# Optimization experiments

Measured on AMD Instinct MI355X. Metric: run time of the kernel, lower is better.

## Reference

```python
import jax, jax.numpy as jnp
import numpy as np

N = 100_000   # active voxels
CIN = 64
COUT = 64
K = 3
L = 128       # voxel grid extent per axis
C = K // 2    # kernel center


def _offsets():
    # spatial offsets (z, y, x) for all non-center kernel taps, in the same
    # enumeration order as the original module's triple loop
    offs = []
    for dz in range(K):
        for dy in range(K):
            for dx in range(K):
                if (dz, dy, dx) != (C, C, C):
                    offs.append((dz - C, dy - C, dx - C))
    return offs


def _build_neighbor_map(coords):
    # coords: [N,3] int, unique. For each offset build (out_idx, in_idx) pairs
    # where voxel out_idx has an active neighbor in_idx at coords+offset.
    keys = (coords[:, 0].astype(np.int64) * L + coords[:, 1]) * L + coords[:, 2]
    order = np.argsort(keys)
    skeys = keys[order]
    pairs = []
    for (z, y, x) in _offsets():
        nb = coords + np.array([z, y, x], dtype=coords.dtype)
        valid = np.all((nb >= 0) & (nb < L), axis=1)
        nkeys = (nb[:, 0].astype(np.int64) * L + nb[:, 1]) * L + nb[:, 2]
        pos = np.clip(np.searchsorted(skeys, nkeys), 0, N - 1)
        found = valid & (skeys[pos] == nkeys)
        out_idx = np.nonzero(found)[0].astype(np.int32)
        in_idx = order[pos[found]].astype(np.int32)
        pairs.append((out_idx, in_idx))
    P = max(len(o) for o, _ in pairs)
    nei = np.zeros((len(pairs), P, 2), dtype=np.int32)
    sizes = np.zeros(len(pairs), dtype=np.int32)
    for i, (o, j) in enumerate(pairs):
        nei[i, :len(o), 0] = o
        nei[i, :len(o), 1] = j
        sizes[i] = len(o)
    return nei, sizes


def setup_inputs() -> dict:
    rng = np.random.default_rng(0)
    flat = rng.choice(L * L * L, size=N, replace=False)  # unique voxel coords
    coords = np.stack([flat // (L * L), (flat // L) % L, flat % L], axis=1).astype(np.int32)
    nei, sizes = _build_neighbor_map(coords)
    key = jax.random.key(0)
    k1, k2, k3 = jax.random.split(key, 3)
    sp_values = jax.random.normal(k1, (N, CIN), dtype=jnp.float32)
    weight = jax.random.normal(k2, (COUT, K, K, K, CIN), dtype=jnp.float32) * 0.05
    bias = jax.random.normal(k3, (COUT,), dtype=jnp.float32)
    return {"sp_values": sp_values, "weight": weight, "bias": bias,
            "nei_indices": jnp.asarray(nei), "nei_sizes": jnp.asarray(sizes)}


def reference(sp_values, weight, bias, nei_indices, nei_sizes):
    # weight: [Cout,kz,ky,kx,Cin] -> [kz,ky,kx,Cin,Cout] (matches torch permute)
    w = jnp.transpose(weight, (1, 2, 3, 4, 0))
    out = sp_values @ w[C, C, C]                                   # center tap: [N,Cout]
    offs = _offsets()
    w_offs = jnp.stack([w[z + C, y + C, x + C] for (z, y, x) in offs])  # [O,Cin,Cout]
    P = nei_indices.shape[1]
    valid = (jnp.arange(P)[None, :] < nei_sizes[:, None]).astype(sp_values.dtype)  # [O,P]
    gathered = sp_values[nei_indices[:, :, 1]] * valid[:, :, None]  # [O,P,Cin], padded rows zeroed
    contrib = jnp.einsum('opc,ocd->opd', gathered, w_offs)          # [O,P,Cout]
    out = out.at[nei_indices[:, :, 0].reshape(-1)].add(contrib.reshape(-1, out.shape[1]))
    return out + bias
```

## Files before the change

### kernel.cpp

```cpp
#include <hip/hip_runtime.h>


typedef __bf16 bf16x8 __attribute__((ext_vector_type(8)));
typedef float f32x4 __attribute__((ext_vector_type(4)));

__device__ __forceinline__ unsigned short f2bf(float f) {
    union { float f; unsigned int u; } v; v.f = f;
    unsigned int u = v.u;
    return (unsigned short)((u + 0x7FFFu + ((u >> 16) & 1u)) >> 16);
}

__device__ __forceinline__ ushort4 cvt4(float4 v) {
    ushort4 b;
    b.x = f2bf(v.x); b.y = f2bf(v.y); b.z = f2bf(v.z); b.w = f2bf(v.w);
    return b;
}

__global__ __launch_bounds__(256) void sp3d_prep(
    const float* __restrict__ sp, const float* __restrict__ w,
    unsigned short* __restrict__ spb, unsigned short* __restrict__ wb,
    int* __restrict__ tbl, int n_rows)
{
    const long gt = (long)blockIdx.x * 256 + threadIdx.x;
    const long stride = (long)gridDim.x * 256;

    const long ntbl = 26L * n_rows;
    for (long i = gt; i < (ntbl >> 2); i += stride)
        *(int4*)&tbl[i * 4] = make_int4(-1, -1, -1, -1);
    if (gt < (ntbl & 3)) tbl[(ntbl & ~3L) + gt] = -1;

    const long nsp = (long)n_rows * 16;
    for (long i = gt; i < nsp; i += stride) {
        float4 v = *(const float4*)&sp[i * 4];
        *(ushort4*)&spb[i * 4] = cvt4(v);
    }

    for (long i = gt; i < 27 * 512; i += stride) {
        int tap = (int)(i >> 9);
        int rem = (int)(i & 511);
        int fragid = rem >> 6, lane = rem & 63;
        int nt = fragid >> 1, half = fragid & 1, ml = lane & 15, quad = lane >> 4;
        const float* src = w + (nt * 16 + ml) * 1728 + tap * 64 + half * 32 + quad * 8;
        float4 v0 = *(const float4*)src;
        float4 v1 = *(const float4*)(src + 4);
        *(ushort4*)&wb[i * 8]     = cvt4(v0);
        *(ushort4*)&wb[i * 8 + 4] = cvt4(v1);
    }
}

__global__ __launch_bounds__(256) void sp3d_build(
    const int* __restrict__ nei, const int* __restrict__ sizes,
    int* __restrict__ tbl, int n_rows, int P)
{
    const int o = blockIdx.y;
    const int p = blockIdx.x * 256 + threadIdx.x;
    if (p < sizes[o]) {
        int2 pr = *(const int2*)&nei[(o * P + p) * 2];
        tbl[(long)o * n_rows + pr.x] = pr.y;
    }
}

__global__ __launch_bounds__(512) void sp3d_main(
    const unsigned short* __restrict__ spb, const unsigned short* __restrict__ wb,
    const float* __restrict__ bias, const int* __restrict__ tbl,
    float* __restrict__ out, int n_rows)
{
    __shared__ unsigned short Bt[2][4096];
    __shared__ int tl[26 * 128];

    const int t = threadIdx.x;
    const int row0 = blockIdx.x * 128;
    const int wid = t >> 6, lane = t & 63, ml = lane & 15, quad = lane >> 4;

    for (int i = t; i < 26 * 128; i += 512) {
        int o = i >> 7;
        int r = row0 + (i & 127);
        tl[i] = tbl[(long)o * n_rows + (r < n_rows ? r : n_rows - 1)];
    }
    *(bf16x8*)&Bt[0][t * 8] = *(const bf16x8*)(wb + t * 8);

    bf16x8 z8;
    #pragma unroll
    for (int j = 0; j < 8; ++j) z8[j] = (__bf16)0.f;

    int curv = tl[wid * 16 + ml];
    bf16x8 a0 = z8, a1 = z8;
    if (curv >= 0) {
        const unsigned short* ap = spb + (long)curv * 64 + quad * 8;
        a0 = *(const bf16x8*)ap;
        a1 = *(const bf16x8*)(ap + 32);
    }

    f32x4 acc[4];
    #pragma unroll
    for (int nt = 0; nt < 4; ++nt) acc[nt] = f32x4{0.f, 0.f, 0.f, 0.f};

    __syncthreads();

    int cur = 0;
    for (int tp = 0; tp < 27; ++tp) {
        bf16x8 s0 = z8;
        if (tp < 26) s0 = *(const bf16x8*)(wb + (tp + 1) * 4096 + t * 8);

        int ninr = -1;
        bf16x8 na0 = z8, na1 = z8;
        if (tp < 26) {
            int tn = tp + 1;
            if (tn == 13) {
                int r = row0 + wid * 16 + ml;
                ninr = (r < n_rows) ? r : n_rows - 1;
            } else {
                int o = tn - (tn > 13 ? 1 : 0);
                ninr = tl[o * 128 + wid * 16 + ml];
            }
            if (ninr >= 0) {
                const unsigned short* ap = spb + (long)ninr * 64 + quad * 8;
                na0 = *(const bf16x8*)ap;
                na1 = *(const bf16x8*)(ap + 32);
            }
        }

        if (__any(curv >= 0)) {
            #pragma unroll
            for (int nt = 0; nt < 4; ++nt) {
                bf16x8 b0 = *(const bf16x8*)&Bt[cur][(nt * 2 + 0) * 512 + lane * 8];
                bf16x8 b1 = *(const bf16x8*)&Bt[cur][(nt * 2 + 1) * 512 + lane * 8];
                acc[nt] = __builtin_amdgcn_mfma_f32_16x16x32_bf16(a0, b0, acc[nt], 0, 0, 0);
                acc[nt] = __builtin_amdgcn_mfma_f32_16x16x32_bf16(a1, b1, acc[nt], 0, 0, 0);
            }
        }

        if (tp < 26) *(bf16x8*)&Bt[cur ^ 1][t * 8] = s0;
        __syncthreads();
        a0 = na0; a1 = na1; curv = ninr;
        cur ^= 1;
    }

    #pragma unroll
    for (int nt = 0; nt < 4; ++nt) {
        int col = nt * 16 + ml;
        float bv = bias[col];
        #pragma unroll
        for (int rg = 0; rg < 4; ++rg) {
            int row = row0 + wid * 16 + quad * 4 + rg;
            if (row < n_rows) out[(long)row * 64 + col] = acc[nt][rg] + bv;
        }
    }
}

extern "C" void kernel_launch(void* const* d_in, const int* in_sizes, int n_in,
                              void* d_out, int out_size, void* d_ws, size_t ws_size,
                              hipStream_t stream) {
    const float* sp    = (const float*)d_in[0];
    const float* w     = (const float*)d_in[1];
    const float* bias  = (const float*)d_in[2];
    const int*   nei   = (const int*)d_in[3];
    const int*   sizes = (const int*)d_in[4];
    float* out = (float*)d_out;

    const int N = in_sizes[0] / 64;
    const int P = in_sizes[3] / (26 * 2);

    char* ws = (char*)d_ws;
    unsigned short* spb = (unsigned short*)ws;
    size_t off = ((size_t)N * 64 * 2 + 255) & ~(size_t)255;
    unsigned short* wb = (unsigned short*)(ws + off);
    off = (off + 27 * 4096 * 2 + 255) & ~(size_t)255;
    int* tbl = (int*)(ws + off);

    sp3d_prep<<<dim3(2048), 256, 0, stream>>>(sp, w, spb, wb, tbl, N);
    sp3d_build<<<dim3((P + 255) / 256, 26), 256, 0, stream>>>(nei, sizes, tbl, N, P);
    sp3d_main<<<dim3((N + 127) / 128), 512, 0, stream>>>(spb, wb, bias, tbl, out, N);
}
```

Before: 133.0 us.

## Split output channels across grid, preload all tap weights to LDS, deepen gather prefetch

The main kernel grid gains a second dimension of 4 that splits the 64 output channels into 16-column blocks. Each block now preloads its slice of all 27 tap weights into shared memory once, which removes the per-tap double-buffered weight loads and __syncthreads. The gathered activation rows are prefetched two taps ahead instead of one. The cost is that every neighbor row is gathered four times, once per channel block, so gather traffic rises fourfold in exchange for more blocks and fewer barriers.

```diff
diff --git a/kernel.cpp b/kernel.cpp
--- a/kernel.cpp
+++ b/kernel.cpp
@@ -65,86 +65,83 @@
     const float* __restrict__ bias, const int* __restrict__ tbl,
     float* __restrict__ out, int n_rows)
 {
-    __shared__ unsigned short Bt[2][4096];
+    __shared__ unsigned short Bt[27 * 1024];
     __shared__ int tl[26 * 128];
 
     const int t = threadIdx.x;
     const int row0 = blockIdx.x * 128;
+    const int cb = blockIdx.y;
     const int wid = t >> 6, lane = t & 63, ml = lane & 15, quad = lane >> 4;
+    const int mrow = wid * 16 + ml;
 
+    for (int j = t; j < 27 * 128; j += 512) {
+        int tap = j >> 7, rem = j & 127;
+        *(bf16x8*)&Bt[j * 8] = *(const bf16x8*)(wb + tap * 4096 + cb * 1024 + rem * 8);
+    }
     for (int i = t; i < 26 * 128; i += 512) {
         int o = i >> 7;
         int r = row0 + (i & 127);
         tl[i] = tbl[(long)o * n_rows + (r < n_rows ? r : n_rows - 1)];
     }
-    *(bf16x8*)&Bt[0][t * 8] = *(const bf16x8*)(wb + t * 8);
+    __syncthreads();
 
     bf16x8 z8;
     #pragma unroll
     for (int j = 0; j < 8; ++j) z8[j] = (__bf16)0.f;
 
-    int curv = tl[wid * 16 + ml];
-    bf16x8 a0 = z8, a1 = z8;
-    if (curv >= 0) {
-        const unsigned short* ap = spb + (long)curv * 64 + quad * 8;
-        a0 = *(const bf16x8*)ap;
-        a1 = *(const bf16x8*)(ap + 32);
+    f32x4 acc = f32x4{0.f, 0.f, 0.f, 0.f};
+
+    int v0, v1;
+    bf16x8 a0 = z8, a1 = z8, na0 = z8, na1 = z8;
+    {
+        v0 = tl[mrow];
+        if (v0 >= 0) {
+            const unsigned short* ap = spb + (long)v0 * 64 + quad * 8;
+            a0 = *(const bf16x8*)ap; a1 = *(const bf16x8*)(ap + 32);
+        }
+        v1 = tl[128 + mrow];
+        if (v1 >= 0) {
+            const unsigned short* ap = spb + (long)v1 * 64 + quad * 8;
+            na0 = *(const bf16x8*)ap; na1 = *(const bf16x8*)(ap + 32);
+        }
     }
 
-    f32x4 acc[4];
     #pragma unroll
-    for (int nt = 0; nt < 4; ++nt) acc[nt] = f32x4{0.f, 0.f, 0.f, 0.f};
-
-    __syncthreads();
-
-    int cur = 0;
     for (int tp = 0; tp < 27; ++tp) {
-        bf16x8 s0 = z8;
-        if (tp < 26) s0 = *(const bf16x8*)(wb + (tp + 1) * 4096 + t * 8);
-
-        int ninr = -1;
-        bf16x8 na0 = z8, na1 = z8;
-        if (tp < 26) {
-            int tn = tp + 1;
+        int v2 = -1;
+        bf16x8 f0 = z8, f1 = z8;
+        if (tp + 2 < 27) {
+            const int tn = tp + 2;
             if (tn == 13) {
-                int r = row0 + wid * 16 + ml;
-                ninr = (r < n_rows) ? r : n_rows - 1;
+                int r = row0 + mrow;
+                v2 = (r < n_rows) ? r : n_rows - 1;
             } else {
-                int o = tn - (tn > 13 ? 1 : 0);
-                ninr = tl[o * 128 + wid * 16 + ml];
+                const int o = tn - (tn > 13 ? 1 : 0);
+                v2 = tl[o * 128 + mrow];
             }
-            if (ninr >= 0) {
-                const unsigned short* ap = spb + (long)ninr * 64 + quad * 8;
-                na0 = *(const bf16x8*)ap;
-                na1 = *(const bf16x8*)(ap + 32);
+            if (v2 >= 0) {
+                const unsigned short* ap = spb + (long)v2 * 64 + quad * 8;
+                f0 = *(const bf16x8*)ap; f1 = *(const bf16x8*)(ap + 32);
             }
         }
 
-        if (__any(curv >= 0)) {
-            #pragma unroll
-            for (int nt = 0; nt < 4; ++nt) {
-                bf16x8 b0 = *(const bf16x8*)&Bt[cur][(nt * 2 + 0) * 512 + lane * 8];
-                bf16x8 b1 = *(const bf16x8*)&Bt[cur][(nt * 2 + 1) * 512 + lane * 8];
-                acc[nt] = __builtin_amdgcn_mfma_f32_16x16x32_bf16(a0, b0, acc[nt], 0, 0, 0);
-                acc[nt] = __builtin_amdgcn_mfma_f32_16x16x32_bf16(a1, b1, acc[nt], 0, 0, 0);
-            }
+        if (__any(v0 >= 0)) {
+            bf16x8 b0 = *(const bf16x8*)&Bt[tp * 1024 + lane * 8];
+            bf16x8 b1 = *(const bf16x8*)&Bt[tp * 1024 + 512 + lane * 8];
+            acc = __builtin_amdgcn_mfma_f32_16x16x32_bf16(a0, b0, acc, 0, 0, 0);
+            acc = __builtin_amdgcn_mfma_f32_16x16x32_bf16(a1, b1, acc, 0, 0, 0);
         }
 
-        if (tp < 26) *(bf16x8*)&Bt[cur ^ 1][t * 8] = s0;
-        __syncthreads();
-        a0 = na0; a1 = na1; curv = ninr;
-        cur ^= 1;
+        v0 = v1; a0 = na0; a1 = na1;
+        v1 = v2; na0 = f0; na1 = f1;
     }
 
+    const int col = cb * 16 + ml;
+    const float bv = bias[col];
     #pragma unroll
-    for (int nt = 0; nt < 4; ++nt) {
-        int col = nt * 16 + ml;
-        float bv = bias[col];
-        #pragma unroll
-        for (int rg = 0; rg < 4; ++rg) {
-            int row = row0 + wid * 16 + quad * 4 + rg;
-            if (row < n_rows) out[(long)row * 64 + col] = acc[nt][rg] + bv;
-        }
+    for (int rg = 0; rg < 4; ++rg) {
+        int row = row0 + wid * 16 + quad * 4 + rg;
+        if (row < n_rows) out[(long)row * 64 + col] = acc[rg] + bv;
     }
 }
 
@@ -170,5 +167,5 @@
 
     sp3d_prep<<<dim3(2048), 256, 0, stream>>>(sp, w, spb, wb, tbl, N);
     sp3d_build<<<dim3((P + 255) / 256, 26), 256, 0, stream>>>(nei, sizes, tbl, N, P);
-    sp3d_main<<<dim3((N + 127) / 128), 512, 0, stream>>>(spb, wb, bias, tbl, out, N);
+    sp3d_main<<<dim3((N + 127) / 128, 4), 512, 0, stream>>>(spb, wb, bias, tbl, out, N);
 }
```

After: 158.2 us. 19.0% more time.
